# Optimization experiments

Hardware: AMD Instinct MI355X
Metric: run time of the kernel (lower is better)

## Reference

```python
import jax, jax.numpy as jnp
import numpy as np

N = 2_000_000   # n_nodes
D = 8           # manifold_dim
C = 1.0         # hyperbolic curvature

# ---- Poincare ball ops (curvature C), vectorized over leading node axis ----
def _hyp_proj(x, eps=1e-5):
    norm = jnp.linalg.norm(x, axis=-1, keepdims=True)
    max_norm = (1.0 - eps) / jnp.sqrt(C)
    return jnp.where(norm > max_norm, x / norm * max_norm, x)

def _mobius_add(x, y):
    xy = jnp.sum(x * y, axis=-1, keepdims=True)
    nx = jnp.sum(x ** 2, axis=-1, keepdims=True)
    ny = jnp.sum(y ** 2, axis=-1, keepdims=True)
    num = (1.0 + 2.0 * C * xy + C * ny) * x + (1.0 - C * nx) * y
    den = 1.0 + 2.0 * C * xy + C ** 2 * nx * ny
    return num / (den + 1e-10)

def _hyp_exp(x, v):
    nv = jnp.maximum(jnp.linalg.norm(v, axis=-1, keepdims=True), 1e-10)
    sc = jnp.sqrt(C)
    nx = jnp.linalg.norm(x, axis=-1, keepdims=True)
    lam = 2.0 / (1.0 - C * nx ** 2)
    coef = jnp.tanh(sc * lam * nv / 2) / (sc * nv)
    return _hyp_proj(_mobius_add(x, coef * v))

def _hyp_log(x, y):
    sub = _mobius_add(-x, y)
    ns = jnp.maximum(jnp.linalg.norm(sub, axis=-1, keepdims=True), 1e-10)
    sc = jnp.sqrt(C)
    nx = jnp.linalg.norm(x, axis=-1, keepdims=True)
    lam = 2.0 / (1.0 - C * nx ** 2)
    coef = jnp.arctanh(sc * ns) / (sc * ns * lam / 2)
    return coef * sub

# ---- sphere ops ----
def _sph_proj(x):
    return x / (jnp.linalg.norm(x, axis=-1, keepdims=True) + 1e-10)

def _sph_log(x, y):
    xy = jnp.clip(jnp.sum(x * y, axis=-1, keepdims=True), -1.0 + 1e-6, 1.0 - 1e-6)
    coef = jnp.arccos(xy) / jnp.sqrt(1.0 - xy ** 2 + 1e-10)
    return coef * (y - xy * x)

def _sph_exp(x, v):
    nv = jnp.maximum(jnp.linalg.norm(v, axis=-1, keepdims=True), 1e-10)
    return _sph_proj(jnp.cos(nv) * x + jnp.sin(nv) * v / nv)


def setup_inputs() -> dict:
    key = jax.random.key(0)
    ks = jax.random.split(key, 9)
    f32 = jnp.float32
    return {
        'features': jax.random.normal(ks[0], (N, 8), dtype=f32),
        # flax Dense default init ~ lecun_normal: std = 1/sqrt(fan_in)
        'W_hyp': jax.random.normal(ks[1], (2, D), dtype=f32) / np.sqrt(2.0),
        'b_hyp': jnp.zeros((D,), dtype=f32),
        'W_spd': jax.random.normal(ks[2], (3, 3), dtype=f32) / np.sqrt(3.0),
        'b_spd': jnp.zeros((3,), dtype=f32),
        'W_sph': jax.random.normal(ks[3], (2, D), dtype=f32) / np.sqrt(2.0),
        'b_sph': jnp.zeros((D,), dtype=f32),
        'W_int': jax.random.normal(ks[4], (4 + D + 3 + D, 32), dtype=f32) / np.sqrt(4.0 + D + 3 + D),
        'b_int': jnp.zeros((32,), dtype=f32),
    }


def reference(features, W_hyp, b_hyp, W_spd, b_spd, W_sph, b_sph, W_int, b_int):
    euclid = features[:, :4]            # [N,4]
    mf = features[:, 4:]                # [N,4] manifold features

    # --- hyperbolic branch: exp-map of MLP output at the origin ---
    hyp_tan = mf[:, 0:2] @ W_hyp + b_hyp            # [N,D]
    hyp_pt = _hyp_exp(jnp.zeros_like(hyp_tan), hyp_tan)

    # --- SPD branch: matrices are diag(exp(Dense(feat)) + 0.1) ---
    spd_diag = jnp.exp(mf[:, 0:3] @ W_spd + b_spd) + 0.1   # [N,3]

    # --- sphere branch ---
    sph_pt = _sph_proj(mf[:, 2:4] @ W_sph + b_sph)          # [N,D]

    # --- geodesic refinement: hyperbolic ---
    hc = _hyp_proj(jnp.mean(hyp_pt, axis=0, keepdims=True))
    hyp_ref = _hyp_exp(hyp_pt, 0.1 * _hyp_log(hyp_pt, hc))

    # --- geodesic refinement: SPD ---
    # matrices and centroid are diagonal, so (1-a)*M + a*centroid is diagonal;
    # eigh + clamp + reconstruct of a diagonal SPD matrix == diag(max(d, 1e-6))
    geo_mean = jnp.exp(jnp.mean(jnp.log(spd_diag + 1e-8), axis=0))   # [3]
    spd_ref_diag = jnp.maximum(0.9 * spd_diag + 0.1 * geo_mean, 1e-6)  # [N,3]
    spd_ref = jnp.eye(3, dtype=spd_ref_diag.dtype) * spd_ref_diag[:, None, :]  # [N,3,3]

    # --- geodesic refinement: sphere ---
    sc = _sph_proj(jnp.mean(sph_pt, axis=0, keepdims=True))
    sph_ref = _sph_exp(sph_pt, 0.1 * _sph_log(sph_pt, sc))

    # --- pullbacks to tangent space + integration ---
    hyp_pull = _hyp_log(jnp.zeros_like(hyp_ref), hyp_ref)
    spd_pull = jnp.log(spd_ref_diag + 1e-8)
    combined = jnp.concatenate([euclid, hyp_pull, spd_pull, sph_ref], axis=-1)  # [N,23]
    integrated = jax.nn.relu(combined @ W_int + b_int)    # [N,32]
    return (integrated, hyp_ref, spd_ref, sph_ref, combined)
```

## Files before the change

kernel.cpp:

```cpp
#include <hip/hip_runtime.h>
#include <math.h>

#define NB1 1024
#define BS  256

__device__ __forceinline__ void compute_base(
    const float4 mf,
    const float* __restrict__ Wh, const float* __restrict__ bh,
    const float* __restrict__ Ws, const float* __restrict__ bs,
    const float* __restrict__ Wp, const float* __restrict__ bp,
    float* hp, float* sd, float* sp)
{
    float ht[8];
    float nv2 = 0.f;
#pragma unroll
    for (int j = 0; j < 8; ++j) {
        float t = mf.x * Wh[j] + mf.y * Wh[8 + j] + bh[j];
        ht[j] = t; nv2 += t * t;
    }
    float nv = fmaxf(sqrtf(nv2), 1e-10f);
    float coef = tanhf(nv) / nv;
    float pn2 = 0.f;
#pragma unroll
    for (int j = 0; j < 8; ++j) {
        float p = coef * ht[j];
        hp[j] = p; pn2 += p * p;
    }
    float pn = sqrtf(pn2);
    if (pn > 0.99999f) {
        float s = 0.99999f / pn;
#pragma unroll
        for (int j = 0; j < 8; ++j) hp[j] *= s;
    }
#pragma unroll
    for (int k = 0; k < 3; ++k) {
        float t = mf.x * Ws[k] + mf.y * Ws[3 + k] + mf.z * Ws[6 + k] + bs[k];
        sd[k] = expf(t) + 0.1f;
    }
    float sl[8]; float sn2 = 0.f;
#pragma unroll
    for (int j = 0; j < 8; ++j) {
        float t = mf.z * Wp[j] + mf.w * Wp[8 + j] + bp[j];
        sl[j] = t; sn2 += t * t;
    }
    float isn = 1.0f / (sqrtf(sn2) + 1e-10f);
#pragma unroll
    for (int j = 0; j < 8; ++j) sp[j] = sl[j] * isn;
}

__global__ __launch_bounds__(BS) void reduce_kernel(
    const float* __restrict__ feat, int n,
    const float* __restrict__ Wh, const float* __restrict__ bh,
    const float* __restrict__ Ws, const float* __restrict__ bs,
    const float* __restrict__ Wp, const float* __restrict__ bp,
    float* __restrict__ partials)
{
    float acc[19];
#pragma unroll
    for (int i = 0; i < 19; ++i) acc[i] = 0.f;
    int stride = gridDim.x * blockDim.x;
    for (int row = blockIdx.x * blockDim.x + threadIdx.x; row < n; row += stride) {
        float4 mf = *(const float4*)(feat + (size_t)row * 8 + 4);
        float hp[8], sd[3], sp[8];
        compute_base(mf, Wh, bh, Ws, bs, Wp, bp, hp, sd, sp);
#pragma unroll
        for (int j = 0; j < 8; ++j) acc[j] += hp[j];
#pragma unroll
        for (int k = 0; k < 3; ++k) acc[8 + k] += logf(sd[k] + 1e-8f);
#pragma unroll
        for (int j = 0; j < 8; ++j) acc[11 + j] += sp[j];
    }
#pragma unroll
    for (int i = 0; i < 19; ++i) {
#pragma unroll
        for (int off = 32; off >= 1; off >>= 1)
            acc[i] += __shfl_down(acc[i], off, 64);
    }
    __shared__ float red[4][19];
    int lane = threadIdx.x & 63, wid = threadIdx.x >> 6;
    if (lane == 0) {
#pragma unroll
        for (int i = 0; i < 19; ++i) red[wid][i] = acc[i];
    }
    __syncthreads();
    if (threadIdx.x < 19) {
        float s = red[0][threadIdx.x] + red[1][threadIdx.x] +
                  red[2][threadIdx.x] + red[3][threadIdx.x];
        partials[(size_t)blockIdx.x * 19 + threadIdx.x] = s;
    }
}

__global__ void finalize_kernel(const float* __restrict__ partials,
                                float* __restrict__ cons, int n)
{
    __shared__ double ms[19];
    int tid = threadIdx.x;
    int k = tid >> 3, w = tid & 7;
    if (k < 19) {
        double s = 0.0;
        for (int b = w; b < NB1; b += 8) s += (double)partials[(size_t)b * 19 + k];
#pragma unroll
        for (int off = 4; off >= 1; off >>= 1) s += __shfl_down(s, off, 8);
        if (w == 0) ms[k] = s / (double)n;
    }
    __syncthreads();
    if (tid == 0) {
        double hn2 = 0.0;
        for (int j = 0; j < 8; ++j) hn2 += ms[j] * ms[j];
        double hn = sqrt(hn2);
        double sch = (hn > 0.99999) ? (0.99999 / hn) : 1.0;
        for (int j = 0; j < 8; ++j) cons[j] = (float)(ms[j] * sch);
        for (int kk = 0; kk < 3; ++kk) cons[8 + kk] = (float)exp(ms[8 + kk]);
        double sn2 = 0.0;
        for (int j = 0; j < 8; ++j) sn2 += ms[11 + j] * ms[11 + j];
        double sn = sqrt(sn2) + 1e-10;
        for (int j = 0; j < 8; ++j) cons[11 + j] = (float)(ms[11 + j] / sn);
    }
}

__global__ __launch_bounds__(BS) void main_kernel(
    const float* __restrict__ feat, int n,
    const float* __restrict__ Wh, const float* __restrict__ bh,
    const float* __restrict__ Ws, const float* __restrict__ bs,
    const float* __restrict__ Wp, const float* __restrict__ bp,
    const float* __restrict__ cons,
    const float* __restrict__ Wi, const float* __restrict__ bi,
    float* __restrict__ out)
{
    int row = blockIdx.x * blockDim.x + threadIdx.x;
    if (row >= n) return;
    size_t r = (size_t)row;
    float4 eu = *(const float4*)(feat + r * 8);
    float4 mf = *(const float4*)(feat + r * 8 + 4);

    float p[8], sd[3], sp[8];
    compute_base(mf, Wh, bh, Ws, bs, Wp, bp, p, sd, sp);

    float hc[8];
#pragma unroll
    for (int j = 0; j < 8; ++j) hc[j] = cons[j];
    float nx2 = 0.f;
#pragma unroll
    for (int j = 0; j < 8; ++j) nx2 += p[j] * p[j];
    float xy = 0.f, ny2 = 0.f;
#pragma unroll
    for (int j = 0; j < 8; ++j) { xy -= p[j] * hc[j]; ny2 += hc[j] * hc[j]; }
    float a1 = 1.f + 2.f * xy + ny2;
    float b1 = 1.f - nx2;
    float id1 = 1.f / (1.f + 2.f * xy + nx2 * ny2 + 1e-10f);
    float sub[8]; float ns2 = 0.f;
#pragma unroll
    for (int j = 0; j < 8; ++j) {
        float s = (a1 * (-p[j]) + b1 * hc[j]) * id1;
        sub[j] = s; ns2 += s * s;
    }
    float ns  = fmaxf(sqrtf(ns2), 1e-10f);
    float lam = 2.f / (1.f - nx2);
    float vcoef = 0.1f * atanhf(ns) / (ns * lam * 0.5f);
    float v[8]; float nv2 = 0.f;
#pragma unroll
    for (int j = 0; j < 8; ++j) { float t = vcoef * sub[j]; v[j] = t; nv2 += t * t; }
    float nvv = fmaxf(sqrtf(nv2), 1e-10f);
    float ecoef = tanhf(lam * nvv * 0.5f) / nvv;
    float y[8]; float xy2 = 0.f, nyy2 = 0.f;
#pragma unroll
    for (int j = 0; j < 8; ++j) { float t = ecoef * v[j]; y[j] = t; xy2 += p[j] * t; nyy2 += t * t; }
    float a2 = 1.f + 2.f * xy2 + nyy2;
    float b2 = 1.f - nx2;
    float id2 = 1.f / (1.f + 2.f * xy2 + nx2 * nyy2 + 1e-10f);
    float hr[8]; float hn2 = 0.f;
#pragma unroll
    for (int j = 0; j < 8; ++j) { float t = (a2 * p[j] + b2 * y[j]) * id2; hr[j] = t; hn2 += t * t; }
    float hn = sqrtf(hn2);
    if (hn > 0.99999f) {
        float s = 0.99999f / hn;
#pragma unroll
        for (int j = 0; j < 8; ++j) hr[j] *= s;
    }
    float nsb2 = 0.f;
#pragma unroll
    for (int j = 0; j < 8; ++j) nsb2 += hr[j] * hr[j];
    float nsb = fmaxf(sqrtf(nsb2), 1e-10f);
    float pcoef = atanhf(nsb) / nsb;

    float scv[8], geo3[3];
#pragma unroll
    for (int j = 0; j < 8; ++j) scv[j] = cons[11 + j];
#pragma unroll
    for (int k = 0; k < 3; ++k) geo3[k] = cons[8 + k];
    float sxy = 0.f;
#pragma unroll
    for (int j = 0; j < 8; ++j) sxy += sp[j] * scv[j];
    sxy = fminf(fmaxf(sxy, -1.f + 1e-6f), 1.f - 1e-6f);
    float svcoef = 0.1f * acosf(sxy) / sqrtf(1.f - sxy * sxy + 1e-10f);
    float sv[8]; float snv2 = 0.f;
#pragma unroll
    for (int j = 0; j < 8; ++j) { float t = svcoef * (scv[j] - sxy * sp[j]); sv[j] = t; snv2 += t * t; }
    float snv = fmaxf(sqrtf(snv2), 1e-10f);
    float cn  = cosf(snv);
    float sn_ = sinf(snv) / snv;
    float st[8]; float stn2 = 0.f;
#pragma unroll
    for (int j = 0; j < 8; ++j) { float t = cn * sp[j] + sn_ * sv[j]; st[j] = t; stn2 += t * t; }
    float istn = 1.f / (sqrtf(stn2) + 1e-10f);
    float sr[8];
#pragma unroll
    for (int j = 0; j < 8; ++j) sr[j] = st[j] * istn;

    float srd[3], spull[3];
#pragma unroll
    for (int k = 0; k < 3; ++k) {
        float t = fmaxf(0.9f * sd[k] + 0.1f * geo3[k], 1e-6f);
        srd[k] = t;
        spull[k] = logf(t + 1e-8f);
    }

    float comb[23];
    comb[0] = eu.x; comb[1] = eu.y; comb[2] = eu.z; comb[3] = eu.w;
#pragma unroll
    for (int j = 0; j < 8; ++j) comb[4 + j] = pcoef * hr[j];
#pragma unroll
    for (int k = 0; k < 3; ++k) comb[12 + k] = spull[k];
#pragma unroll
    for (int j = 0; j < 8; ++j) comb[15 + j] = sr[j];

    float* out_int = out;
    float* out_hyp = out + (size_t)n * 32;
    float* out_spd = out + (size_t)n * 40;
    float* out_sph = out + (size_t)n * 49;
    float* out_cmb = out + (size_t)n * 57;

    *(float4*)(out_hyp + r * 8)     = make_float4(hr[0], hr[1], hr[2], hr[3]);
    *(float4*)(out_hyp + r * 8 + 4) = make_float4(hr[4], hr[5], hr[6], hr[7]);
    {
        float* os = out_spd + r * 9;
        os[0] = srd[0]; os[1] = 0.f; os[2] = 0.f;
        os[3] = 0.f;    os[4] = srd[1]; os[5] = 0.f;
        os[6] = 0.f;    os[7] = 0.f;   os[8] = srd[2];
    }
    *(float4*)(out_sph + r * 8)     = make_float4(sr[0], sr[1], sr[2], sr[3]);
    *(float4*)(out_sph + r * 8 + 4) = make_float4(sr[4], sr[5], sr[6], sr[7]);
    {
        float* oc = out_cmb + r * 23;
#pragma unroll
        for (int k2 = 0; k2 < 23; ++k2) oc[k2] = comb[k2];
    }
#pragma unroll
    for (int j0 = 0; j0 < 32; j0 += 4) {
        float a_[4];
#pragma unroll
        for (int jj = 0; jj < 4; ++jj) {
            float acc = bi[j0 + jj];
#pragma unroll
            for (int k2 = 0; k2 < 23; ++k2) acc += comb[k2] * Wi[k2 * 32 + j0 + jj];
            a_[jj] = fmaxf(acc, 0.f);
        }
        *(float4*)(out_int + r * 32 + j0) = make_float4(a_[0], a_[1], a_[2], a_[3]);
    }
}

extern "C" void kernel_launch(void* const* d_in, const int* in_sizes, int n_in,
                              void* d_out, int out_size, void* d_ws, size_t ws_size,
                              hipStream_t stream) {
    const float* feat = (const float*)d_in[0];
    const float* Wh = (const float*)d_in[1];
    const float* bh = (const float*)d_in[2];
    const float* Ws = (const float*)d_in[3];
    const float* bs = (const float*)d_in[4];
    const float* Wp = (const float*)d_in[5];
    const float* bp = (const float*)d_in[6];
    const float* Wi = (const float*)d_in[7];
    const float* bi = (const float*)d_in[8];
    int n = in_sizes[0] / 8;

    float* partials = (float*)d_ws;
    float* cons = partials + NB1 * 19;
    float* out = (float*)d_out;

    reduce_kernel<<<NB1, BS, 0, stream>>>(feat, n, Wh, bh, Ws, bs, Wp, bp, partials);
    finalize_kernel<<<1, 256, 0, stream>>>(partials, cons, n);
    main_kernel<<<(n + BS - 1) / BS, BS, 0, stream>>>(feat, n, Wh, bh, Ws, bs, Wp, bp,
                                                      cons, Wi, bi, out);
}
```

Baseline: 816.0 us.

## Stage per-row outputs through shared memory for coalesced global stores

Each thread's output rows (integrated, combined, SPD, hyperbolic, sphere) are written to padded LDS buffers, and then the block copies them out with consecutive threads writing consecutive global addresses. This targets strided per-thread stores, most of all the 23-float and 9-float rows, which coalesce poorly. The cost is several block barriers, about 33 KB of LDS per block that may limit occupancy, and scalar rather than float4 stores.

```diff
diff --git a/kernel.cpp b/kernel.cpp
--- a/kernel.cpp
+++ b/kernel.cpp
@@ -127,102 +127,12 @@
     const float* __restrict__ Wi, const float* __restrict__ bi,
     float* __restrict__ out)
 {
-    int row = blockIdx.x * blockDim.x + threadIdx.x;
-    if (row >= n) return;
-    size_t r = (size_t)row;
-    float4 eu = *(const float4*)(feat + r * 8);
-    float4 mf = *(const float4*)(feat + r * 8 + 4);
-
-    float p[8], sd[3], sp[8];
-    compute_base(mf, Wh, bh, Ws, bs, Wp, bp, p, sd, sp);
-
-    float hc[8];
-#pragma unroll
-    for (int j = 0; j < 8; ++j) hc[j] = cons[j];
-    float nx2 = 0.f;
-#pragma unroll
-    for (int j = 0; j < 8; ++j) nx2 += p[j] * p[j];
-    float xy = 0.f, ny2 = 0.f;
-#pragma unroll
-    for (int j = 0; j < 8; ++j) { xy -= p[j] * hc[j]; ny2 += hc[j] * hc[j]; }
-    float a1 = 1.f + 2.f * xy + ny2;
-    float b1 = 1.f - nx2;
-    float id1 = 1.f / (1.f + 2.f * xy + nx2 * ny2 + 1e-10f);
-    float sub[8]; float ns2 = 0.f;
-#pragma unroll
-    for (int j = 0; j < 8; ++j) {
-        float s = (a1 * (-p[j]) + b1 * hc[j]) * id1;
-        sub[j] = s; ns2 += s * s;
-    }
-    float ns  = fmaxf(sqrtf(ns2), 1e-10f);
-    float lam = 2.f / (1.f - nx2);
-    float vcoef = 0.1f * atanhf(ns) / (ns * lam * 0.5f);
-    float v[8]; float nv2 = 0.f;
-#pragma unroll
-    for (int j = 0; j < 8; ++j) { float t = vcoef * sub[j]; v[j] = t; nv2 += t * t; }
-    float nvv = fmaxf(sqrtf(nv2), 1e-10f);
-    float ecoef = tanhf(lam * nvv * 0.5f) / nvv;
-    float y[8]; float xy2 = 0.f, nyy2 = 0.f;
-#pragma unroll
-    for (int j = 0; j < 8; ++j) { float t = ecoef * v[j]; y[j] = t; xy2 += p[j] * t; nyy2 += t * t; }
-    float a2 = 1.f + 2.f * xy2 + nyy2;
-    float b2 = 1.f - nx2;
-    float id2 = 1.f / (1.f + 2.f * xy2 + nx2 * nyy2 + 1e-10f);
-    float hr[8]; float hn2 = 0.f;
-#pragma unroll
-    for (int j = 0; j < 8; ++j) { float t = (a2 * p[j] + b2 * y[j]) * id2; hr[j] = t; hn2 += t * t; }
-    float hn = sqrtf(hn2);
-    if (hn > 0.99999f) {
-        float s = 0.99999f / hn;
-#pragma unroll
-        for (int j = 0; j < 8; ++j) hr[j] *= s;
-    }
-    float nsb2 = 0.f;
-#pragma unroll
-    for (int j = 0; j < 8; ++j) nsb2 += hr[j] * hr[j];
-    float nsb = fmaxf(sqrtf(nsb2), 1e-10f);
-    float pcoef = atanhf(nsb) / nsb;
-
-    float scv[8], geo3[3];
-#pragma unroll
-    for (int j = 0; j < 8; ++j) scv[j] = cons[11 + j];
-#pragma unroll
-    for (int k = 0; k < 3; ++k) geo3[k] = cons[8 + k];
-    float sxy = 0.f;
-#pragma unroll
-    for (int j = 0; j < 8; ++j) sxy += sp[j] * scv[j];
-    sxy = fminf(fmaxf(sxy, -1.f + 1e-6f), 1.f - 1e-6f);
-    float svcoef = 0.1f * acosf(sxy) / sqrtf(1.f - sxy * sxy + 1e-10f);
-    float sv[8]; float snv2 = 0.f;
-#pragma unroll
-    for (int j = 0; j < 8; ++j) { float t = svcoef * (scv[j] - sxy * sp[j]); sv[j] = t; snv2 += t * t; }
-    float snv = fmaxf(sqrtf(snv2), 1e-10f);
-    float cn  = cosf(snv);
-    float sn_ = sinf(snv) / snv;
-    float st[8]; float stn2 = 0.f;
-#pragma unroll
-    for (int j = 0; j < 8; ++j) { float t = cn * sp[j] + sn_ * sv[j]; st[j] = t; stn2 += t * t; }
-    float istn = 1.f / (sqrtf(stn2) + 1e-10f);
-    float sr[8];
-#pragma unroll
-    for (int j = 0; j < 8; ++j) sr[j] = st[j] * istn;
-
-    float srd[3], spull[3];
-#pragma unroll
-    for (int k = 0; k < 3; ++k) {
-        float t = fmaxf(0.9f * sd[k] + 0.1f * geo3[k], 1e-6f);
-        srd[k] = t;
-        spull[k] = logf(t + 1e-8f);
-    }
-
-    float comb[23];
-    comb[0] = eu.x; comb[1] = eu.y; comb[2] = eu.z; comb[3] = eu.w;
-#pragma unroll
-    for (int j = 0; j < 8; ++j) comb[4 + j] = pcoef * hr[j];
-#pragma unroll
-    for (int k = 0; k < 3; ++k) comb[12 + k] = spull[k];
-#pragma unroll
-    for (int j = 0; j < 8; ++j) comb[15 + j] = sr[j];
+    __shared__ float sbuf[BS * 33];
+    const int tid = threadIdx.x;
+    const int blockStart = blockIdx.x * BS;
+    const int row = blockStart + tid;
+    const bool valid = row < n;
+    const int vr = min(BS, n - blockStart);
 
     float* out_int = out;
     float* out_hyp = out + (size_t)n * 32;
@@ -230,32 +140,152 @@
     float* out_sph = out + (size_t)n * 49;
     float* out_cmb = out + (size_t)n * 57;
 
-    *(float4*)(out_hyp + r * 8)     = make_float4(hr[0], hr[1], hr[2], hr[3]);
-    *(float4*)(out_hyp + r * 8 + 4) = make_float4(hr[4], hr[5], hr[6], hr[7]);
+    float comb[23], hr[8], srd[3], sr[8];
+
+    if (valid) {
+        size_t r = (size_t)row;
+        float4 eu = *(const float4*)(feat + r * 8);
+        float4 mf = *(const float4*)(feat + r * 8 + 4);
+
+        float p[8], sd[3], sp[8];
+        compute_base(mf, Wh, bh, Ws, bs, Wp, bp, p, sd, sp);
+
+        float hc[8];
+#pragma unroll
+        for (int j = 0; j < 8; ++j) hc[j] = cons[j];
+        float nx2 = 0.f;
+#pragma unroll
+        for (int j = 0; j < 8; ++j) nx2 += p[j] * p[j];
+        float xy = 0.f, ny2 = 0.f;
+#pragma unroll
+        for (int j = 0; j < 8; ++j) { xy -= p[j] * hc[j]; ny2 += hc[j] * hc[j]; }
+        float a1 = 1.f + 2.f * xy + ny2;
+        float b1 = 1.f - nx2;
+        float id1 = 1.f / (1.f + 2.f * xy + nx2 * ny2 + 1e-10f);
+        float sub[8]; float ns2 = 0.f;
+#pragma unroll
+        for (int j = 0; j < 8; ++j) {
+            float s = (a1 * (-p[j]) + b1 * hc[j]) * id1;
+            sub[j] = s; ns2 += s * s;
+        }
+        float ns  = fmaxf(sqrtf(ns2), 1e-10f);
+        float lam = 2.f / (1.f - nx2);
+        float vcoef = 0.1f * atanhf(ns) / (ns * lam * 0.5f);
+        float v[8]; float nv2 = 0.f;
+#pragma unroll
+        for (int j = 0; j < 8; ++j) { float t = vcoef * sub[j]; v[j] = t; nv2 += t * t; }
+        float nvv = fmaxf(sqrtf(nv2), 1e-10f);
+        float ecoef = tanhf(lam * nvv * 0.5f) / nvv;
+        float y[8]; float xy2 = 0.f, nyy2 = 0.f;
+#pragma unroll
+        for (int j = 0; j < 8; ++j) { float t = ecoef * v[j]; y[j] = t; xy2 += p[j] * t; nyy2 += t * t; }
+        float a2 = 1.f + 2.f * xy2 + nyy2;
+        float b2 = 1.f - nx2;
+        float id2 = 1.f / (1.f + 2.f * xy2 + nx2 * nyy2 + 1e-10f);
+        float hn2 = 0.f;
+#pragma unroll
+        for (int j = 0; j < 8; ++j) { float t = (a2 * p[j] + b2 * y[j]) * id2; hr[j] = t; hn2 += t * t; }
+        float hn = sqrtf(hn2);
+        if (hn > 0.99999f) {
+            float s = 0.99999f / hn;
+#pragma unroll
+            for (int j = 0; j < 8; ++j) hr[j] *= s;
+        }
+        float nsb2 = 0.f;
+#pragma unroll
+        for (int j = 0; j < 8; ++j) nsb2 += hr[j] * hr[j];
+        float nsb = fmaxf(sqrtf(nsb2), 1e-10f);
+        float pcoef = atanhf(nsb) / nsb;
+
+        float scv[8], geo3[3];
+#pragma unroll
+        for (int j = 0; j < 8; ++j) scv[j] = cons[11 + j];
+#pragma unroll
+        for (int k = 0; k < 3; ++k) geo3[k] = cons[8 + k];
+        float sxy = 0.f;
+#pragma unroll
+        for (int j = 0; j < 8; ++j) sxy += sp[j] * scv[j];
+        sxy = fminf(fmaxf(sxy, -1.f + 1e-6f), 1.f - 1e-6f);
+        float svcoef = 0.1f * acosf(sxy) / sqrtf(1.f - sxy * sxy + 1e-10f);
+        float sv[8]; float snv2 = 0.f;
+#pragma unroll
+        for (int j = 0; j < 8; ++j) { float t = svcoef * (scv[j] - sxy * sp[j]); sv[j] = t; snv2 += t * t; }
+        float snv = fmaxf(sqrtf(snv2), 1e-10f);
+        float cn  = cosf(snv);
+        float sn_ = sinf(snv) / snv;
+        float st[8]; float stn2 = 0.f;
+#pragma unroll
+        for (int j = 0; j < 8; ++j) { float t = cn * sp[j] + sn_ * sv[j]; st[j] = t; stn2 += t * t; }
+        float istn = 1.f / (sqrtf(stn2) + 1e-10f);
+#pragma unroll
+        for (int j = 0; j < 8; ++j) sr[j] = st[j] * istn;
+
+#pragma unroll
+        for (int k = 0; k < 3; ++k)
+            srd[k] = fmaxf(0.9f * sd[k] + 0.1f * geo3[k], 1e-6f);
+
+        comb[0] = eu.x; comb[1] = eu.y; comb[2] = eu.z; comb[3] = eu.w;
+#pragma unroll
+        for (int j = 0; j < 8; ++j) comb[4 + j] = pcoef * hr[j];
+#pragma unroll
+        for (int k = 0; k < 3; ++k) comb[12 + k] = logf(srd[k] + 1e-8f);
+#pragma unroll
+        for (int j = 0; j < 8; ++j) comb[15 + j] = sr[j];
+    }
+
+    if (valid) {
+        float* lrow = sbuf + tid * 33;
+#pragma unroll
+        for (int j = 0; j < 32; ++j) {
+            float acc = bi[j];
+#pragma unroll
+            for (int k2 = 0; k2 < 23; ++k2) acc += comb[k2] * Wi[k2 * 32 + j];
+            lrow[j] = fmaxf(acc, 0.f);
+        }
+    }
+    __syncthreads();
     {
-        float* os = out_spd + r * 9;
-        os[0] = srd[0]; os[1] = 0.f; os[2] = 0.f;
-        os[3] = 0.f;    os[4] = srd[1]; os[5] = 0.f;
-        os[6] = 0.f;    os[7] = 0.f;   os[8] = srd[2];
-    }
-    *(float4*)(out_sph + r * 8)     = make_float4(sr[0], sr[1], sr[2], sr[3]);
-    *(float4*)(out_sph + r * 8 + 4) = make_float4(sr[4], sr[5], sr[6], sr[7]);
+        float* dst = out_int + (size_t)blockStart * 32;
+        const int E = vr * 32;
+        for (int i = tid; i < E; i += BS) dst[i] = sbuf[(i >> 5) * 33 + (i & 31)];
+    }
+    __syncthreads();
+
+    if (valid) {
+        float* lrow = sbuf + tid * 23;
+#pragma unroll
+        for (int k = 0; k < 23; ++k) lrow[k] = comb[k];
+    }
+    __syncthreads();
     {
-        float* oc = out_cmb + r * 23;
-#pragma unroll
-        for (int k2 = 0; k2 < 23; ++k2) oc[k2] = comb[k2];
-    }
-#pragma unroll
-    for (int j0 = 0; j0 < 32; j0 += 4) {
-        float a_[4];
-#pragma unroll
-        for (int jj = 0; jj < 4; ++jj) {
-            float acc = bi[j0 + jj];
-#pragma unroll
-            for (int k2 = 0; k2 < 23; ++k2) acc += comb[k2] * Wi[k2 * 32 + j0 + jj];
-            a_[jj] = fmaxf(acc, 0.f);
-        }
-        *(float4*)(out_int + r * 32 + j0) = make_float4(a_[0], a_[1], a_[2], a_[3]);
+        float* dst = out_cmb + (size_t)blockStart * 23;
+        const int E = vr * 23;
+        for (int i = tid; i < E; i += BS) dst[i] = sbuf[i];
+    }
+    __syncthreads();
+
+    if (valid) {
+        float* ls = sbuf + tid * 9;
+        ls[0] = srd[0]; ls[1] = 0.f;    ls[2] = 0.f;
+        ls[3] = 0.f;    ls[4] = srd[1]; ls[5] = 0.f;
+        ls[6] = 0.f;    ls[7] = 0.f;    ls[8] = srd[2];
+        float* lh = sbuf + BS * 9 + tid * 9;
+#pragma unroll
+        for (int j = 0; j < 8; ++j) lh[j] = hr[j];
+        float* lp = sbuf + 2 * BS * 9 + tid * 9;
+#pragma unroll
+        for (int j = 0; j < 8; ++j) lp[j] = sr[j];
+    }
+    __syncthreads();
+    {
+        float* d1 = out_spd + (size_t)blockStart * 9;
+        int E = vr * 9;
+        for (int i = tid; i < E; i += BS) d1[i] = sbuf[i];
+        float* d2 = out_hyp + (size_t)blockStart * 8;
+        E = vr * 8;
+        for (int i = tid; i < E; i += BS) d2[i] = sbuf[BS * 9 + (i >> 3) * 9 + (i & 7)];
+        float* d3 = out_sph + (size_t)blockStart * 8;
+        for (int i = tid; i < E; i += BS) d3[i] = sbuf[2 * BS * 9 + (i >> 3) * 9 + (i & 7)];
     }
 }
 
```

After: 735.9 us. 1.11x faster.
